# Performance work log

Measured on AMD Instinct MI355X. Metric: run time of the kernel, lower is better.

The kernel has to match this reference:

```python
import jax, jax.numpy as jnp
import numpy as np

N_EMBD = 2048
N_HEAD = 16
N_KV_HEAD = 4
HD = N_EMBD // N_HEAD  # 128
B, T = 1, 4096
EPS = 1e-6


def apply_rope(x, cos, sin):
    # x: [B,T,H,hd]; cos/sin: [T,1,hd//2]
    hd = x.shape[-1] // 2
    x1, x2 = x[..., :hd], x[..., hd:]
    y1 = x1 * cos + x2 * sin
    y2 = x2 * cos - x1 * sin
    return jnp.concatenate((y1, y2), axis=-1).astype(x.dtype)


def rms_norm(x, eps=EPS):
    return x * jax.lax.rsqrt(jnp.mean(jnp.square(x), axis=-1, keepdims=True) + eps)


def setup_inputs() -> dict:
    key = jax.random.key(0)
    ks = jax.random.split(key, 7)
    s = 0.02
    return {
        "x": jax.random.normal(ks[0], (B, T, N_EMBD), dtype=jnp.float32),
        "cos": jax.random.normal(ks[1], (T, 1, HD // 2), dtype=jnp.float32),
        "sin": jax.random.normal(ks[2], (T, 1, HD // 2), dtype=jnp.float32),
        "wq": jax.random.normal(ks[3], (N_EMBD, N_HEAD * HD), dtype=jnp.float32) * s,
        "wk": jax.random.normal(ks[4], (N_EMBD, N_KV_HEAD * HD), dtype=jnp.float32) * s,
        "wv": jax.random.normal(ks[5], (N_EMBD, N_KV_HEAD * HD), dtype=jnp.float32) * s,
        "wo": jax.random.normal(ks[6], (N_EMBD, N_EMBD), dtype=jnp.float32) * s,
    }


def reference(x, cos, sin, wq, wk, wv, wo):
    Bb, Tt, C = x.shape
    q = (x @ wq).reshape(Bb, Tt, N_HEAD, HD)
    k = (x @ wk).reshape(Bb, Tt, N_KV_HEAD, HD)
    v = (x @ wv).reshape(Bb, Tt, N_KV_HEAD, HD)
    q = rms_norm(apply_rope(q, cos, sin))
    k = rms_norm(apply_rope(k, cos, sin))
    g = N_HEAD // N_KV_HEAD
    if g > 1:
        k = jnp.repeat(k, g, axis=2)  # [B,T,H,hd]
        v = jnp.repeat(v, g, axis=2)
    scale = 1.0 / jnp.sqrt(jnp.float32(HD))
    # scores: [B,H,T,S]
    scores = jnp.einsum("bthd,bshd->bhts", q, k) * scale
    causal = jnp.tril(jnp.ones((Tt, Tt), dtype=bool))
    scores = jnp.where(causal, scores, jnp.finfo(scores.dtype).min)
    attn = jax.nn.softmax(scores, axis=-1)
    y = jnp.einsum("bhts,bshd->bthd", attn, v).reshape(Bb, Tt, C)
    return y @ wo
```

## Files before the change

kernel.cpp:

```cpp
#include <hip/hip_runtime.h>

#define T_SEQ 4096
#define C_EMB 2048
#define NH 16
#define NKV 4
#define HD 128

typedef short bf16x8 __attribute__((ext_vector_type(8)));
typedef float f32x4 __attribute__((ext_vector_type(4)));
typedef unsigned short u16x4 __attribute__((ext_vector_type(4)));

__device__ inline unsigned short f2bf(float f) {
    unsigned int u = __float_as_uint(f);
    unsigned int r = (u + 0x7FFFu + ((u >> 16) & 1u)) >> 16;
    return (unsigned short)r;
}

__device__ __forceinline__ void async_cp16(const unsigned short* g, unsigned short* l) {
    __builtin_amdgcn_global_load_lds((const __attribute__((address_space(1))) unsigned int*)g,
                                     (__attribute__((address_space(3))) unsigned int*)l,
                                     16, 0, 0);
}

__global__ __launch_bounds__(256) void cvt_bf16(const float* __restrict__ in,
                                                unsigned short* __restrict__ out, int n) {
    int i = (blockIdx.x * 256 + threadIdx.x) * 4;
    if (i >= n) return;
    float4 f = *(const float4*)(&in[i]);
    u16x4 o;
    o.x = f2bf(f.x); o.y = f2bf(f.y); o.z = f2bf(f.z); o.w = f2bf(f.w);
    *(u16x4*)(&out[i]) = o;
}

__global__ __launch_bounds__(256) void transpose_all(const float* __restrict__ wq,
                                                     const float* __restrict__ wk,
                                                     const float* __restrict__ wv,
                                                     const float* __restrict__ wo,
                                                     unsigned short* __restrict__ wqkvT,
                                                     unsigned short* __restrict__ woT) {
    __shared__ float tile[32][33];
    int z = blockIdx.z;
    const float* in;
    unsigned short* out;
    int ld_in;
    if (z == 0)      { in = wq; out = wqkvT;                         ld_in = 2048; }
    else if (z == 1) { in = wk; out = wqkvT + (size_t)2048 * 2048;   ld_in = 512;  }
    else if (z == 2) { in = wv; out = wqkvT + (size_t)2560 * 2048;   ld_in = 512;  }
    else             { in = wo; out = woT;                           ld_in = 2048; }
    if ((z == 1 || z == 2) && blockIdx.x >= 16) return;

    int x = blockIdx.x * 32 + threadIdx.x;
    for (int i = threadIdx.y; i < 32; i += 8) {
        int y = blockIdx.y * 32 + i;
        tile[i][threadIdx.x] = in[(size_t)y * ld_in + x];
    }
    __syncthreads();
    int xo = blockIdx.y * 32 + threadIdx.x;
    for (int i = threadIdx.y; i < 32; i += 8) {
        int yo = blockIdx.x * 32 + i;
        out[(size_t)yo * 2048 + xo] = f2bf(tile[threadIdx.x][i]);
    }
}

__global__ __launch_bounds__(256, 3) void gemm_qkv(const unsigned short* __restrict__ A,
                                                   const unsigned short* __restrict__ Bt,
                                                   const float* __restrict__ cosb,
                                                   const float* __restrict__ sinb,
                                                   unsigned short* __restrict__ Qn,
                                                   unsigned short* __restrict__ Kn,
                                                   unsigned short* __restrict__ Vt) {
    __shared__ __align__(16) unsigned short As[3][128 * 32];
    __shared__ __align__(16) unsigned short Bs[3][128 * 32];
    const int K = 2048;
    int t = threadIdx.x;
    int w = t >> 6, lane = t & 63;
    int ln = lane & 15, q = lane >> 4;
    int wm = w * 32;

    int d = blockIdx.y * 24 + blockIdx.x;
    int xcd = d & 7, l = d >> 3;
    int lx = l % 12, ly = l / 12;
    int bx = (xcd & 1) * 12 + lx;
    int by = (xcd >> 1) * 8 + ly;
    int m0 = by * 128, n0 = bx * 128;

    f32x4 acc[2][8] = {};

    int r0 = t >> 2, c0 = (t & 3) ^ ((t >> 4) & 3);
    int L1 = 256 + t;
    int r1 = L1 >> 2, c1 = (L1 & 3) ^ ((L1 >> 4) & 3);
    const unsigned short* a0 = &A[(size_t)(m0 + r0) * K + c0 * 8];
    const unsigned short* a1 = &A[(size_t)(m0 + r1) * K + c1 * 8];
    const unsigned short* b0 = &Bt[(size_t)(n0 + r0) * K + c0 * 8];
    const unsigned short* b1 = &Bt[(size_t)(n0 + r1) * K + c1 * 8];

    auto stage = [&](int b, int k0) {
        async_cp16(a0 + k0, &As[b][w * 512]);
        async_cp16(a1 + k0, &As[b][2048 + w * 512]);
        async_cp16(b0 + k0, &Bs[b][w * 512]);
        async_cp16(b1 + k0, &Bs[b][2048 + w * 512]);
    };

    stage(0, 0);
    stage(1, 32);

    int bc = 0;
    for (int it = 0; it < 64; ++it) {
        if (it < 63) asm volatile("s_waitcnt vmcnt(4)" ::: "memory");
        else         asm volatile("s_waitcnt vmcnt(0)" ::: "memory");
        __builtin_amdgcn_s_barrier();
        __builtin_amdgcn_sched_barrier(0);
        if (it < 62) {
            int bn = bc + 2; if (bn >= 3) bn -= 3;
            stage(bn, (it + 2) * 32);
        }
        int cs = (q ^ ((ln >> 2) & 3)) * 8;
        bf16x8 af[2], bfr[8];
#pragma unroll
        for (int i = 0; i < 2; ++i) af[i] = *(const bf16x8*)(&As[bc][(wm + i * 16 + ln) * 32 + cs]);
#pragma unroll
        for (int j = 0; j < 8; ++j) bfr[j] = *(const bf16x8*)(&Bs[bc][(j * 16 + ln) * 32 + cs]);
#pragma unroll
        for (int i = 0; i < 2; ++i)
#pragma unroll
            for (int j = 0; j < 8; ++j)
                acc[i][j] = __builtin_amdgcn_mfma_f32_16x16x32_bf16(af[i], bfr[j], acc[i][j], 0, 0, 0);
        bc = (bc == 2) ? 0 : bc + 1;
    }

    if (n0 < 2560) {
        bool isQ = (n0 < 2048);
        int h = isQ ? (n0 >> 7) : ((n0 - 2048) >> 7);
#pragma unroll
        for (int i = 0; i < 2; ++i)
#pragma unroll
            for (int r = 0; r < 4; ++r) {
                int row = m0 + wm + i * 16 + q * 4 + r;
                float y1[4], y2[4];
                float ss = 0.0f;
#pragma unroll
                for (int j = 0; j < 4; ++j) {
                    float a = acc[i][j][r];
                    float b = acc[i][j + 4][r];
                    float cc = cosb[row * 64 + j * 16 + ln];
                    float sv = sinb[row * 64 + j * 16 + ln];
                    y1[j] = a * cc + b * sv;
                    y2[j] = b * cc - a * sv;
                    ss += y1[j] * y1[j] + y2[j] * y2[j];
                }
                ss += __shfl_xor(ss, 1);
                ss += __shfl_xor(ss, 2);
                ss += __shfl_xor(ss, 4);
                ss += __shfl_xor(ss, 8);
                float rv = rsqrtf(ss * (1.0f / 128.0f) + 1e-6f);
                if (isQ) {
                    float s = rv * (0.08838834764831845f * 1.4426950408889634f);
                    unsigned short* ob = Qn + (size_t)row * 2048 + h * 128;
#pragma unroll
                    for (int j = 0; j < 4; ++j) {
                        ob[j * 16 + ln] = f2bf(y1[j] * s);
                        ob[64 + j * 16 + ln] = f2bf(y2[j] * s);
                    }
                } else {
                    unsigned short* ob = Kn + (size_t)row * 512 + h * 128;
#pragma unroll
                    for (int j = 0; j < 4; ++j) {
                        ob[j * 16 + ln] = f2bf(y1[j] * rv);
                        ob[64 + j * 16 + ln] = f2bf(y2[j] * rv);
                    }
                }
            }
    } else {
        int v0 = n0 - 2560;
        unsigned short* sm = &As[0][0];
#pragma unroll
        for (int half = 0; half < 2; ++half) {
            __syncthreads();
#pragma unroll
            for (int i = 0; i < 2; ++i)
#pragma unroll
                for (int jj = 0; jj < 4; ++jj) {
                    int j = half * 4 + jj;
                    int cc = jj * 16 + ln;
                    int rr = wm + i * 16 + q * 4;
                    u16x4 pk;
                    pk.x = f2bf(acc[i][j][0]); pk.y = f2bf(acc[i][j][1]);
                    pk.z = f2bf(acc[i][j][2]); pk.w = f2bf(acc[i][j][3]);
                    *(u16x4*)(&sm[cc * 136 + rr]) = pk;
                }
            __syncthreads();
            int vtr = t >> 2, mseg = (t & 3) * 32;
            unsigned short* dst = Vt + (size_t)(v0 + half * 64 + vtr) * 4096 + m0 + mseg;
            const unsigned short* src = &sm[vtr * 136 + mseg];
            *(int4*)(dst)      = *(const int4*)(src);
            *(int4*)(dst + 8)  = *(const int4*)(src + 8);
            *(int4*)(dst + 16) = *(const int4*)(src + 16);
            *(int4*)(dst + 24) = *(const int4*)(src + 24);
        }
    }
}

__global__ __launch_bounds__(256, 3) void gemm_bt_db(const unsigned short* __restrict__ A,
                                                     const unsigned short* __restrict__ Bt,
                                                     float* __restrict__ C, int M, int N, int K) {
    __shared__ __align__(16) unsigned short As[3][128 * 32];
    __shared__ __align__(16) unsigned short Bs[3][128 * 32];
    int t = threadIdx.x;
    int w = t >> 6, lane = t & 63;
    int ln = lane & 15, q = lane >> 4;
    int wm = (w >> 1) * 64, wn = (w & 1) * 64;

    int d = blockIdx.y * 16 + blockIdx.x;
    int xcd = d & 7, l = d >> 3;
    int lx = l & 7, ly = l >> 3;
    int bx = (xcd & 1) * 8 + lx;
    int by = (xcd >> 1) * 8 + ly;
    int m0 = by * 128, n0 = bx * 128;

    f32x4 acc[4][4] = {};

    int r0 = t >> 2, c0 = (t & 3) ^ ((t >> 4) & 3);
    int L1 = 256 + t;
    int r1 = L1 >> 2, c1 = (L1 & 3) ^ ((L1 >> 4) & 3);
    const unsigned short* a0 = &A[(size_t)(m0 + r0) * K + c0 * 8];
    const unsigned short* a1 = &A[(size_t)(m0 + r1) * K + c1 * 8];
    const unsigned short* b0 = &Bt[(size_t)(n0 + r0) * K + c0 * 8];
    const unsigned short* b1 = &Bt[(size_t)(n0 + r1) * K + c1 * 8];

    auto stage = [&](int b, int k0) {
        async_cp16(a0 + k0, &As[b][w * 512]);
        async_cp16(a1 + k0, &As[b][2048 + w * 512]);
        async_cp16(b0 + k0, &Bs[b][w * 512]);
        async_cp16(b1 + k0, &Bs[b][2048 + w * 512]);
    };

    stage(0, 0);
    stage(1, 32);

    int niter = K >> 5;
    int bc = 0;
    for (int it = 0; it < niter; ++it) {
        if (it < niter - 1) asm volatile("s_waitcnt vmcnt(4)" ::: "memory");
        else                asm volatile("s_waitcnt vmcnt(0)" ::: "memory");
        __builtin_amdgcn_s_barrier();
        __builtin_amdgcn_sched_barrier(0);
        if (it < niter - 2) {
            int bn = bc + 2; if (bn >= 3) bn -= 3;
            stage(bn, (it + 2) * 32);
        }
        int cs = (q ^ ((ln >> 2) & 3)) * 8;
        bf16x8 af[4], bfr[4];
#pragma unroll
        for (int i = 0; i < 4; ++i) af[i] = *(const bf16x8*)(&As[bc][(wm + i * 16 + ln) * 32 + cs]);
#pragma unroll
        for (int j = 0; j < 4; ++j) bfr[j] = *(const bf16x8*)(&Bs[bc][(wn + j * 16 + ln) * 32 + cs]);
#pragma unroll
        for (int i = 0; i < 4; ++i)
#pragma unroll
            for (int j = 0; j < 4; ++j)
                acc[i][j] = __builtin_amdgcn_mfma_f32_16x16x32_bf16(af[i], bfr[j], acc[i][j], 0, 0, 0);
        bc = (bc == 2) ? 0 : bc + 1;
    }
#pragma unroll
    for (int i = 0; i < 4; ++i)
#pragma unroll
        for (int j = 0; j < 4; ++j)
#pragma unroll
            for (int r = 0; r < 4; ++r) {
                int row = m0 + wm + i * 16 + q * 4 + r;
                int col = n0 + wn + j * 16 + ln;
                C[(size_t)row * N + col] = acc[i][j][r];
            }
}

__global__ __launch_bounds__(256) void flash_attn(const unsigned short* __restrict__ Qn,
                                                  const unsigned short* __restrict__ Kn,
                                                  const unsigned short* __restrict__ Vt,
                                                  unsigned short* __restrict__ Ao) {
    __shared__ __align__(16) unsigned short Ks[2][64 * 128];
    __shared__ __align__(16) unsigned short Vs[2][128 * 64];
    __shared__ __align__(16) unsigned short Pl[4][16 * 72];

    int pairi = blockIdx.x;
    int h = blockIdx.y;
    int kvh = h >> 2;
    int t = threadIdx.x;
    int w = t >> 6, lane = t & 63;
    int ln = lane & 15, q = lane >> 4;

    int nA = 64 - pairi;
    int bq = 63 - pairi;
    int wq0 = bq * 64 + w * 16;

    bf16x8 qf[4];
    {
        const unsigned short* qb = Qn + (size_t)(wq0 + ln) * 2048 + h * 128;
#pragma unroll
        for (int kc = 0; kc < 4; ++kc) qf[kc] = *(const bf16x8*)(qb + kc * 32 + q * 8);
    }

    f32x4 o[8] = {};
    f32x4 l_p = {0.f, 0.f, 0.f, 0.f};

    const unsigned short* kbase[4];
    const unsigned short* vbase[4];
#pragma unroll
    for (int s = 0; s < 4; ++s) {
        int L = s * 256 + t;
        int key = L >> 4;
        int ck = (L & 15) ^ (key & 15);
        kbase[s] = Kn + (size_t)key * 512 + kvh * 128 + ck * 8;
        int hd = L >> 3;
        int cv = (L & 7) ^ (hd & 7);
        vbase[s] = Vt + (size_t)(kvh * 128 + hd) * 4096 + cv * 8;
    }

#pragma unroll
    for (int s = 0; s < 4; ++s) async_cp16(kbase[s], &Ks[0][s * 2048 + w * 512]);
#pragma unroll
    for (int s = 0; s < 4; ++s) async_cp16(vbase[s], &Vs[0][s * 2048 + w * 512]);

    for (int it = 0; it < 65; ++it) {
        __syncthreads();

        int nxt = it + 1;
        if (nxt < 65) {
            int nkt = (nxt < nA) ? nxt * 64 : (nxt - nA) * 64;
            size_t koff = (size_t)nkt * 512;
            unsigned short* kd = Ks[nxt & 1];
            unsigned short* vd = Vs[nxt & 1];
#pragma unroll
            for (int s = 0; s < 4; ++s) async_cp16(kbase[s] + koff, kd + s * 2048 + w * 512);
#pragma unroll
            for (int s = 0; s < 4; ++s) async_cp16(vbase[s] + nkt, vd + s * 2048 + w * 512);
        }

        if (it == nA) {
#pragma unroll
            for (int r = 0; r < 4; ++r) {
                float lsum = l_p[r];
                lsum += __shfl_xor(lsum, 1);
                lsum += __shfl_xor(lsum, 2);
                lsum += __shfl_xor(lsum, 4);
                lsum += __shfl_xor(lsum, 8);
                float inv = 1.0f / lsum;
                int row = wq0 + q * 4 + r;
                unsigned short* ob = Ao + (size_t)row * 2048 + h * 128;
#pragma unroll
                for (int f = 0; f < 8; ++f) ob[f * 16 + ln] = f2bf(o[f][r] * inv);
            }
            bq = pairi;
            wq0 = bq * 64 + w * 16;
            const unsigned short* qb = Qn + (size_t)(wq0 + ln) * 2048 + h * 128;
#pragma unroll
            for (int kc = 0; kc < 4; ++kc) qf[kc] = *(const bf16x8*)(qb + kc * 32 + q * 8);
#pragma unroll
            for (int f = 0; f < 8; ++f) o[f] = (f32x4){0.f, 0.f, 0.f, 0.f};
            l_p = (f32x4){0.f, 0.f, 0.f, 0.f};
        }

        int kt0 = (it < nA) ? it * 64 : (it - nA) * 64;
        const unsigned short* kb = Ks[it & 1];
        const unsigned short* vb = Vs[it & 1];

        f32x4 sA[4] = {{-16.6f, -16.6f, -16.6f, -16.6f}, {-16.6f, -16.6f, -16.6f, -16.6f},
                       {-16.6f, -16.6f, -16.6f, -16.6f}, {-16.6f, -16.6f, -16.6f, -16.6f}};
        __builtin_amdgcn_s_setprio(1);
#pragma unroll
        for (int jt = 0; jt < 4; ++jt) {
            int key = jt * 16 + ln;
#pragma unroll
            for (int kc = 0; kc < 4; ++kc) {
                int cs = ((kc * 4 + q) ^ ln) * 8;
                bf16x8 kf = *(const bf16x8*)(&kb[key * 128 + cs]);
                sA[jt] = __builtin_amdgcn_mfma_f32_16x16x32_bf16(qf[kc], kf, sA[jt], 0, 0, 0);
            }
        }
        __builtin_amdgcn_s_setprio(0);
        if (kt0 + 63 > wq0) {
#pragma unroll
            for (int jt = 0; jt < 4; ++jt)
#pragma unroll
                for (int r = 0; r < 4; ++r) {
                    int key = kt0 + jt * 16 + ln;
                    int row = wq0 + q * 4 + r;
                    if (key > row) sA[jt][r] = -3e38f;
                }
        }
#pragma unroll
        for (int r = 0; r < 4; ++r) {
            int prow = (q * 4 + r) * 72;
#pragma unroll
            for (int jt = 0; jt < 4; ++jt) {
                float p = __builtin_amdgcn_exp2f(sA[jt][r]);
                Pl[w][prow + jt * 16 + ln] = (unsigned short)(__float_as_uint(p) >> 16);
                l_p[r] += p;
            }
        }

        __builtin_amdgcn_s_setprio(1);
#pragma unroll
        for (int ks = 0; ks < 2; ++ks) {
            bf16x8 pa = *(const bf16x8*)(&Pl[w][ln * 72 + ks * 32 + q * 8]);
            int cs = ((ks * 4 + q) ^ (ln & 7)) * 8;
#pragma unroll
            for (int f = 0; f < 8; ++f) {
                bf16x8 vf = *(const bf16x8*)(&vb[(f * 16 + ln) * 64 + cs]);
                o[f] = __builtin_amdgcn_mfma_f32_16x16x32_bf16(pa, vf, o[f], 0, 0, 0);
            }
        }
        __builtin_amdgcn_s_setprio(0);
    }
#pragma unroll
    for (int r = 0; r < 4; ++r) {
        float lsum = l_p[r];
        lsum += __shfl_xor(lsum, 1);
        lsum += __shfl_xor(lsum, 2);
        lsum += __shfl_xor(lsum, 4);
        lsum += __shfl_xor(lsum, 8);
        float inv = 1.0f / lsum;
        int row = wq0 + q * 4 + r;
        unsigned short* ob = Ao + (size_t)row * 2048 + h * 128;
#pragma unroll
        for (int f = 0; f < 8; ++f) ob[f * 16 + ln] = f2bf(o[f][r] * inv);
    }
}

extern "C" void kernel_launch(void* const* d_in, const int* in_sizes, int n_in,
                              void* d_out, int out_size, void* d_ws, size_t ws_size,
                              hipStream_t stream) {
    const float* x    = (const float*)d_in[0];
    const float* cosb = (const float*)d_in[1];
    const float* sinb = (const float*)d_in[2];
    const float* wq   = (const float*)d_in[3];
    const float* wk   = (const float*)d_in[4];
    const float* wv   = (const float*)d_in[5];
    const float* wo   = (const float*)d_in[6];
    float* out = (float*)d_out;

    char* ws = (char*)d_ws;
    unsigned short* xb    = (unsigned short*)ws;
    unsigned short* wqkvT = xb    + (size_t)4096 * 2048;
    unsigned short* woT   = wqkvT + (size_t)3072 * 2048;
    unsigned short* Qn    = woT   + (size_t)2048 * 2048;
    unsigned short* Kn    = Qn    + (size_t)4096 * 2048;
    unsigned short* Vt    = Kn    + (size_t)4096 * 512;
    unsigned short* Ao    = Vt    + (size_t)512 * 4096;

    cvt_bf16<<<(4096 * 2048 / 4 + 255) / 256, 256, 0, stream>>>(x, xb, 4096 * 2048);
    transpose_all<<<dim3(64, 64, 4), dim3(32, 8), 0, stream>>>(wq, wk, wv, wo, wqkvT, woT);
    gemm_qkv<<<dim3(24, 32), 256, 0, stream>>>(xb, wqkvT, cosb, sinb, Qn, Kn, Vt);
    flash_attn<<<dim3(32, 16), 256, 0, stream>>>(Qn, Kn, Vt, Ao);
    gemm_bt_db<<<dim3(16, 32), 256, 0, stream>>>(Ao, woT, out, 4096, 2048, 2048);
}
```

Before: 350.4 us.

## Replace output projection GEMM with 256x256 tile, 512-thread double-buffered kernel

The final projection GEMM now uses 256x256 block tiles with 8 waves, a K-step of 64 with XOR-swizzled LDS, and double buffering instead of 128x128 triple-buffered tiles. This raises data reuse per block and cuts global/LDS traffic per FLOP. The grid shrinks to 128 blocks, which may underfill the CUs, and the XCD-aware block remapping is removed.

```diff
diff --git a/kernel.cpp b/kernel.cpp
--- a/kernel.cpp
+++ b/kernel.cpp
@@ -200,75 +200,75 @@
     }
 }
 
-__global__ __launch_bounds__(256, 3) void gemm_bt_db(const unsigned short* __restrict__ A,
-                                                     const unsigned short* __restrict__ Bt,
-                                                     float* __restrict__ C, int M, int N, int K) {
-    __shared__ __align__(16) unsigned short As[3][128 * 32];
-    __shared__ __align__(16) unsigned short Bs[3][128 * 32];
+__global__ __launch_bounds__(512, 2) void gemm_bt_256(const unsigned short* __restrict__ A,
+                                                      const unsigned short* __restrict__ Bt,
+                                                      float* __restrict__ C, int M, int N, int K) {
+    __shared__ __align__(16) unsigned short As[2][256 * 64];
+    __shared__ __align__(16) unsigned short Bs[2][256 * 64];
     int t = threadIdx.x;
     int w = t >> 6, lane = t & 63;
     int ln = lane & 15, q = lane >> 4;
-    int wm = (w >> 1) * 64, wn = (w & 1) * 64;
-
-    int d = blockIdx.y * 16 + blockIdx.x;
-    int xcd = d & 7, l = d >> 3;
-    int lx = l & 7, ly = l >> 3;
-    int bx = (xcd & 1) * 8 + lx;
-    int by = (xcd >> 1) * 8 + ly;
-    int m0 = by * 128, n0 = bx * 128;
-
-    f32x4 acc[4][4] = {};
-
-    int r0 = t >> 2, c0 = (t & 3) ^ ((t >> 4) & 3);
-    int L1 = 256 + t;
-    int r1 = L1 >> 2, c1 = (L1 & 3) ^ ((L1 >> 4) & 3);
-    const unsigned short* a0 = &A[(size_t)(m0 + r0) * K + c0 * 8];
-    const unsigned short* a1 = &A[(size_t)(m0 + r1) * K + c1 * 8];
-    const unsigned short* b0 = &Bt[(size_t)(n0 + r0) * K + c0 * 8];
-    const unsigned short* b1 = &Bt[(size_t)(n0 + r1) * K + c1 * 8];
+    int wr = w >> 2, wc = w & 3;
+    int m0 = blockIdx.y * 256, n0 = blockIdx.x * 256;
+
+    f32x4 acc[8][4] = {};
+
+    const unsigned short* ab[4];
+    const unsigned short* bb[4];
+#pragma unroll
+    for (int s = 0; s < 4; ++s) {
+        int L = s * 512 + t;
+        int r = L >> 3;
+        int c = (L & 7) ^ (r & 7);
+        ab[s] = &A[(size_t)(m0 + r) * K + c * 8];
+        bb[s] = &Bt[(size_t)(n0 + r) * K + c * 8];
+    }
 
     auto stage = [&](int b, int k0) {
-        async_cp16(a0 + k0, &As[b][w * 512]);
-        async_cp16(a1 + k0, &As[b][2048 + w * 512]);
-        async_cp16(b0 + k0, &Bs[b][w * 512]);
-        async_cp16(b1 + k0, &Bs[b][2048 + w * 512]);
+#pragma unroll
+        for (int s = 0; s < 4; ++s) {
+            async_cp16(ab[s] + k0, &As[b][s * 4096 + w * 512]);
+            async_cp16(bb[s] + k0, &Bs[b][s * 4096 + w * 512]);
+        }
     };
 
     stage(0, 0);
-    stage(1, 32);
-
-    int niter = K >> 5;
-    int bc = 0;
-    for (int it = 0; it < niter; ++it) {
-        if (it < niter - 1) asm volatile("s_waitcnt vmcnt(4)" ::: "memory");
-        else                asm volatile("s_waitcnt vmcnt(0)" ::: "memory");
+    asm volatile("s_waitcnt vmcnt(0)" ::: "memory");
+    __builtin_amdgcn_s_barrier();
+
+    int buf = 0;
+    for (int it = 0; it < 32; ++it) {
+        if (it < 31) stage(buf ^ 1, (it + 1) * 64);
+#pragma unroll
+        for (int kk = 0; kk < 2; ++kk) {
+            bf16x8 bfr[4];
+#pragma unroll
+            for (int j = 0; j < 4; ++j) {
+                int row = wc * 64 + j * 16 + ln;
+                bfr[j] = *(const bf16x8*)(&Bs[buf][row * 64 + (((kk * 4 + q) ^ (row & 7)) * 8)]);
+            }
+#pragma unroll
+            for (int i = 0; i < 8; ++i) {
+                int row = wr * 128 + i * 16 + ln;
+                bf16x8 a = *(const bf16x8*)(&As[buf][row * 64 + (((kk * 4 + q) ^ (row & 7)) * 8)]);
+#pragma unroll
+                for (int j = 0; j < 4; ++j)
+                    acc[i][j] = __builtin_amdgcn_mfma_f32_16x16x32_bf16(a, bfr[j], acc[i][j], 0, 0, 0);
+            }
+        }
+        asm volatile("s_waitcnt vmcnt(0)" ::: "memory");
         __builtin_amdgcn_s_barrier();
-        __builtin_amdgcn_sched_barrier(0);
-        if (it < niter - 2) {
-            int bn = bc + 2; if (bn >= 3) bn -= 3;
-            stage(bn, (it + 2) * 32);
-        }
-        int cs = (q ^ ((ln >> 2) & 3)) * 8;
-        bf16x8 af[4], bfr[4];
-#pragma unroll
-        for (int i = 0; i < 4; ++i) af[i] = *(const bf16x8*)(&As[bc][(wm + i * 16 + ln) * 32 + cs]);
-#pragma unroll
-        for (int j = 0; j < 4; ++j) bfr[j] = *(const bf16x8*)(&Bs[bc][(wn + j * 16 + ln) * 32 + cs]);
-#pragma unroll
-        for (int i = 0; i < 4; ++i)
-#pragma unroll
-            for (int j = 0; j < 4; ++j)
-                acc[i][j] = __builtin_amdgcn_mfma_f32_16x16x32_bf16(af[i], bfr[j], acc[i][j], 0, 0, 0);
-        bc = (bc == 2) ? 0 : bc + 1;
-    }
-#pragma unroll
-    for (int i = 0; i < 4; ++i)
+        buf ^= 1;
+    }
+
+#pragma unroll
+    for (int i = 0; i < 8; ++i)
 #pragma unroll
         for (int j = 0; j < 4; ++j)
 #pragma unroll
             for (int r = 0; r < 4; ++r) {
-                int row = m0 + wm + i * 16 + q * 4 + r;
-                int col = n0 + wn + j * 16 + ln;
+                int row = m0 + wr * 128 + i * 16 + q * 4 + r;
+                int col = n0 + wc * 64 + j * 16 + ln;
                 C[(size_t)row * N + col] = acc[i][j][r];
             }
 }
@@ -451,5 +451,5 @@
     transpose_all<<<dim3(64, 64, 4), dim3(32, 8), 0, stream>>>(wq, wk, wv, wo, wqkvT, woT);
     gemm_qkv<<<dim3(24, 32), 256, 0, stream>>>(xb, wqkvT, cosb, sinb, Qn, Kn, Vt);
     flash_attn<<<dim3(32, 16), 256, 0, stream>>>(Qn, Kn, Vt, Ao);
-    gemm_bt_db<<<dim3(16, 32), 256, 0, stream>>>(Ao, woT, out, 4096, 2048, 2048);
-}
+    gemm_bt_256<<<dim3(8, 16), 512, 0, stream>>>(Ao, woT, out, 4096, 2048, 2048);
+}
```

New measurement: 371.9 us. 1.06x slower.
